# Optimization experiments

Hardware: AMD Instinct MI355X
Metric: run time of the kernel (lower is better)

The kernel has to match this reference:

```python
import jax, jax.numpy as jnp
import numpy as np

B, N, D, H = 2, 2048, 1024, 16
DK = D // H
SCALE = DK ** -0.5


def setup_inputs() -> dict:
    key = jax.random.key(0)
    ks = jax.random.split(key, 11)
    s = D ** -0.5
    return {
        "q": jax.random.normal(ks[0], (B, N, D), jnp.float32),
        "k": jax.random.normal(ks[1], (B, N, D), jnp.float32),
        "v": jax.random.normal(ks[2], (B, N, D), jnp.float32),
        "Wq": jax.random.normal(ks[3], (D, D), jnp.float32) * s,
        "bq": jnp.zeros((D,), jnp.float32),
        "Wk": jax.random.normal(ks[4], (D, D), jnp.float32) * s,
        "bk": jnp.zeros((D,), jnp.float32),
        "Wv": jax.random.normal(ks[5], (D, D), jnp.float32) * s,
        "bv": jnp.zeros((D,), jnp.float32),
        "Wo": jax.random.normal(ks[6], (D, D), jnp.float32) * s,
        "bo": jnp.zeros((D,), jnp.float32),
    }


def _split_heads(x):
    # [b, n, h*d] -> [b, h, n, d]
    b, n, _ = x.shape
    return x.reshape(b, n, H, DK).transpose(0, 2, 1, 3)


def reference(q, k, v, Wq, bq, Wk, bk, Wv, bv, Wo, bo):
    qh = _split_heads(q @ Wq.T + bq)
    kh = _split_heads(k @ Wk.T + bk)
    vh = _split_heads(v @ Wv.T + bv)
    dots = jnp.einsum('bhid,bhjd->bhij', qh, kh) * SCALE
    attn = jax.nn.softmax(dots, axis=-1)
    out = jnp.einsum('bhij,bhjd->bhid', attn, vh)
    out = out.transpose(0, 2, 1, 3).reshape(q.shape[0], q.shape[1], D)
    return out @ Wo.T + bo
```

## Files before the change

kernel.cpp:

```cpp
#include <hip/hip_runtime.h>
#include <hip/hip_bf16.h>
#include <cstdint>
#include <cstddef>

#define BB 2
#define NN 2048
#define DD 1024
#define HH 16
#define DKK 64
#define SCALE 0.125f
#define LOG2E 1.4426950408889634f

typedef __bf16 bf16;
typedef __bf16 bf16x4 __attribute__((ext_vector_type(4)));
typedef __bf16 bf16x8 __attribute__((ext_vector_type(8)));
typedef float f32x4 __attribute__((ext_vector_type(4)));
typedef short s16x4 __attribute__((ext_vector_type(4)));

#define GLD(gp, lp)                                                            \
  __builtin_amdgcn_global_load_lds(                                            \
      (const __attribute__((address_space(1))) void*)(gp),                     \
      (__attribute__((address_space(3))) void*)(lp), 16, 0, 0)

struct CvtArgs { const float* s[7]; bf16* d[7]; int n[7]; };

__global__ void k_cvt(CvtArgs a) {
  const int seg = blockIdx.y;
  const float* __restrict__ s = a.s[seg];
  bf16* __restrict__ d = a.d[seg];
  int i = (blockIdx.x * 256 + threadIdx.x) * 8;
  if (i >= a.n[seg]) return;
  float4 f0 = *(const float4*)(s + i);
  float4 f1 = *(const float4*)(s + i + 4);
  bf16x8 o;
  o[0] = (bf16)f0.x; o[1] = (bf16)f0.y; o[2] = (bf16)f0.z; o[3] = (bf16)f0.w;
  o[4] = (bf16)f1.x; o[5] = (bf16)f1.y; o[6] = (bf16)f1.z; o[7] = (bf16)f1.w;
  *(bf16x8*)(d + i) = o;
}

template <int BN>
__device__ __forceinline__ void gemm_body(
    const bf16* __restrict__ A, const bf16* __restrict__ W,
    const float* __restrict__ bias, bf16* __restrict__ outB,
    float* __restrict__ outF, int mode, float oscale, int m0, int n0) {
  const int K = 1024;
  constexpr int NI = BN / 32;
  constexpr int BI = BN * 8 / 256;
  __shared__ bf16 lA[128 * 64];
  __shared__ bf16 lB[BN * 64];
  const int t = threadIdx.x;
  const int lane = t & 63, quad = lane >> 4, l16 = lane & 15, w = t >> 6;
  const int wm = (w >> 1) * 64, wn = (w & 1) * (BN / 2);

  f32x4 acc[4][NI] = {};

  const bf16* gA[4]; const bf16* gB[BI];
#pragma unroll
  for (int i4 = 0; i4 < 4; i4++) {
    int i = i4 * 256 + t;
    int r = i >> 3, c = (i & 7) ^ (r & 7);
    gA[i4] = A + (size_t)(m0 + r) * K + c * 8;
  }
#pragma unroll
  for (int i4 = 0; i4 < BI; i4++) {
    int i = i4 * 256 + t;
    int r = i >> 3, c = (i & 7) ^ (r & 7);
    gB[i4] = W + (size_t)(n0 + r) * K + c * 8;
  }

  for (int kb = 0; kb < K; kb += 64) {
    __syncthreads();
#pragma unroll
    for (int i4 = 0; i4 < 4; i4++) GLD(gA[i4] + kb, lA + (i4 * 256 + t) * 8);
#pragma unroll
    for (int i4 = 0; i4 < BI; i4++) GLD(gB[i4] + kb, lB + (i4 * 256 + t) * 8);
    __syncthreads();

#pragma unroll
    for (int kb2 = 0; kb2 < 2; kb2++) {
      bf16x8 af[4], bfr[NI];
      const int ch = ((kb2 * 4 + quad) ^ (l16 & 7)) * 8;
#pragma unroll
      for (int i = 0; i < 4; i++)
        af[i] = *(const bf16x8*)(lA + (wm + i * 16 + l16) * 64 + ch);
#pragma unroll
      for (int i = 0; i < NI; i++)
        bfr[i] = *(const bf16x8*)(lB + (wn + i * 16 + l16) * 64 + ch);
#pragma unroll
      for (int mi = 0; mi < 4; mi++)
#pragma unroll
        for (int ni = 0; ni < NI; ni++)
          acc[mi][ni] = __builtin_amdgcn_mfma_f32_16x16x32_bf16(
              af[mi], bfr[ni], acc[mi][ni], 0, 0, 0);
    }
  }

  if (mode == 2) {
    __syncthreads();
    bf16* scr = (w < 2 ? lA : lB) + (w & 1) * 4096;
#pragma unroll
    for (int ni = 0; ni < NI; ni++) {
      int c = ni * 16 + l16;
      float bs = bias[n0 + wn + c];
#pragma unroll
      for (int mi = 0; mi < 4; mi++) {
        int u = (mi * 2 + (quad >> 1)) ^ (c & 7);
        bf16x4 pv;
#pragma unroll
        for (int r = 0; r < 4; r++)
          pv[r] = (bf16)((acc[mi][ni][r] + bs) * oscale);
        *(bf16x4*)(scr + c * 64 + u * 8 + (quad & 1) * 4) = pv;
      }
    }
    __syncthreads();
    {
      const int gm0 = m0 + wm;
      const int b = gm0 >> 11, row0 = gm0 & 2047;
#pragma unroll
      for (int it = 0; it < 8; it++) {
        int c = it * 8 + (lane >> 3);
        int u = (lane & 7) ^ (lane >> 3);
        bf16x8 val = *(const bf16x8*)(scr + c * 64 + u * 8);
        int gn = n0 + wn + c;
        int h = gn >> 6, dk = gn & 63;
        *(bf16x8*)(outB + ((size_t)(b * HH + h) * DKK + dk) * NN + row0 +
                   (lane & 7) * 8) = val;
      }
    }
    return;
  }
#pragma unroll
  for (int mi = 0; mi < 4; mi++) {
#pragma unroll
    for (int ni = 0; ni < NI; ni++) {
#pragma unroll
      for (int r = 0; r < 4; r++) {
        int gm = m0 + wm + mi * 16 + quad * 4 + r;
        int gn = n0 + wn + ni * 16 + l16;
        float v = (acc[mi][ni][r] + bias[gn]) * oscale;
        if (mode == 3) {
          outF[(size_t)gm * 1024 + gn] = v;
        } else {
          int b = gm >> 11, row = gm & 2047;
          int h = gn >> 6, dk = gn & 63;
          outB[((size_t)(b * HH + h) * NN + row) * DKK + dk] = (bf16)v;
        }
      }
    }
  }
}

struct QkvArgs {
  const bf16* A; const bf16* W; const float* b[3]; bf16* o[3]; float sc0;
};

__global__ __launch_bounds__(256, 3) void k_qkv(QkvArgs g) {
  const int z = blockIdx.z;
  gemm_body<128>(g.A + (size_t)z * 4194304, g.W + (size_t)z * 1048576,
                 g.b[z], g.o[z], nullptr, z == 2 ? 2 : 0,
                 z == 0 ? g.sc0 : 1.0f, blockIdx.x * 128, blockIdx.y * 128);
}

__global__ __launch_bounds__(256, 4) void k_oproj(
    const bf16* __restrict__ A, const bf16* __restrict__ W,
    const float* __restrict__ bias, float* __restrict__ out) {
  gemm_body<64>(A, W, bias, nullptr, out, 3, 1.0f, blockIdx.x * 128,
                blockIdx.y * 64);
}

__global__ __launch_bounds__(512, 4) void k_attn(
    const bf16* __restrict__ Qp, const bf16* __restrict__ Kp,
    const bf16* __restrict__ Vt, bf16* __restrict__ Ao) {
  __shared__ bf16 lK[2][128 * 64];
  __shared__ bf16 lV[2][64 * 128];
  const int t = threadIdx.x;
  const int lane = t & 63, quad = lane >> 4, l16 = lane & 15, w = t >> 6;
  const int wq = w & 3;
  const int kh = w >> 2;
  const int bh = blockIdx.x;
  const int qt = blockIdx.y;
  const bf16* Qb = Qp + (size_t)bh * NN * DKK;
  const bf16* Kb = Kp + (size_t)bh * NN * DKK;
  const bf16* Vb = Vt + (size_t)bh * DKK * NN;

  const int qr0 = qt * 128 + wq * 32;
  bf16x8 qf[2][2];
#pragma unroll
  for (int j = 0; j < 2; j++)
#pragma unroll
    for (int kq = 0; kq < 2; kq++)
      qf[j][kq] = *(const bf16x8*)(Qb + (size_t)(qr0 + j * 16 + l16) * DKK +
                                   kq * 32 + quad * 8);

  float lj[2] = {0.f, 0.f};
  f32x4 oaccT[2][4] = {};

  const bf16* gK[2]; const bf16* gV[2];
#pragma unroll
  for (int i2 = 0; i2 < 2; i2++) {
    int i = i2 * 512 + t;
    int rK = i >> 3, cK = (i & 7) ^ (rK & 7);
    gK[i2] = Kb + (size_t)rK * DKK + cK * 8;
    int rV = i >> 4, cV = (i & 15) ^ (rV & 15);
    gV[i2] = Vb + (size_t)rV * NN + cV * 8;
  }
  const int swzK0 = (quad ^ (l16 & 7)) * 8;
  const int swzK1 = ((4 + quad) ^ (l16 & 7)) * 8;

#pragma unroll
  for (int i2 = 0; i2 < 2; i2++) {
    GLD(gK[i2], &lK[0][(i2 * 512 + t) * 8]);
    GLD(gV[i2], &lV[0][(i2 * 512 + t) * 8]);
  }

  int p = 0;
  for (int kt = 0; kt < NN; kt += 128) {
    __syncthreads();
    if (kt + 128 < NN) {
#pragma unroll
      for (int i2 = 0; i2 < 2; i2++) {
        GLD(gK[i2] + (size_t)(kt + 128) * DKK, &lK[p ^ 1][(i2 * 512 + t) * 8]);
        GLD(gV[i2] + (kt + 128), &lV[p ^ 1][(i2 * 512 + t) * 8]);
      }
    }

    f32x4 s[2][4];
#pragma unroll
    for (int tt = 0; tt < 4; tt++) {
      const bf16* kbase = &lK[p][((kh * 4 + tt) * 16 + l16) * 64];
      bf16x8 kf0 = *(const bf16x8*)(kbase + swzK0);
      bf16x8 kf1 = *(const bf16x8*)(kbase + swzK1);
#pragma unroll
      for (int j = 0; j < 2; j++) {
        f32x4 z = {0.f, 0.f, 0.f, 0.f};
        z = __builtin_amdgcn_mfma_f32_16x16x32_bf16(kf0, qf[j][0], z, 0, 0, 0);
        z = __builtin_amdgcn_mfma_f32_16x16x32_bf16(kf1, qf[j][1], z, 0, 0, 0);
        s[j][tt] = z;
      }
    }

    s16x4 pa[2][4];
#pragma unroll
    for (int j = 0; j < 2; j++) {
      float rs = 0.f;
#pragma unroll
      for (int tt = 0; tt < 4; tt++) {
        bf16x4 pb;
#pragma unroll
        for (int r = 0; r < 4; r++) {
          float pe = __builtin_amdgcn_exp2f(s[j][tt][r]);
          rs += pe;
          pb[r] = (bf16)pe;
        }
        pa[j][tt] = __builtin_bit_cast(s16x4, pb);
      }
      lj[j] += rs;
    }

#pragma unroll
    for (int tt = 0; tt < 4; tt++) {
#pragma unroll
      for (int ni = 0; ni < 4; ni++) {
        int rv = ni * 16 + l16;
        int cc = kh * 8 + 2 * tt + (quad >> 1);
        const bf16* vaddr =
            &lV[p][rv * 128 + ((cc ^ l16) * 8) + (quad & 1) * 4];
        s16x4 vb = __builtin_bit_cast(s16x4, *(const bf16x4*)vaddr);
#pragma unroll
        for (int j = 0; j < 2; j++)
          oaccT[j][ni] = __builtin_amdgcn_mfma_f32_16x16x16bf16_1k(
              vb, pa[j][tt], oaccT[j][ni], 0, 0, 0);
      }
    }
    p ^= 1;
  }

  __syncthreads();
  float* redO = (float*)&lK[0][0];
  float* redL = (float*)&lV[0][0];
  const int R = wq * 64 + lane;
  if (kh == 1) {
#pragma unroll
    for (int j = 0; j < 2; j++)
#pragma unroll
      for (int ni = 0; ni < 4; ni++)
        *(f32x4*)(redO + ((j * 4 + ni) * 1024 + R * 4)) = oaccT[j][ni];
    redL[R * 2 + 0] = lj[0];
    redL[R * 2 + 1] = lj[1];
  }
  __syncthreads();
  if (kh == 0) {
#pragma unroll
    for (int j = 0; j < 2; j++)
#pragma unroll
      for (int ni = 0; ni < 4; ni++)
        oaccT[j][ni] += *(const f32x4*)(redO + ((j * 4 + ni) * 1024 + R * 4));
    lj[0] += redL[R * 2 + 0];
    lj[1] += redL[R * 2 + 1];

    const int b = bh >> 4, h = bh & 15;
#pragma unroll
    for (int j = 0; j < 2; j++) {
      float l = lj[j];
      l += __shfl_xor(l, 16);
      l += __shfl_xor(l, 32);
      const float inv = 1.0f / l;
      bf16* dst = Ao + ((size_t)(b * NN) + qr0 + j * 16 + l16) * DD +
                  h * DKK + quad * 4;
#pragma unroll
      for (int ni = 0; ni < 4; ni++) {
        bf16x4 ov;
#pragma unroll
        for (int r = 0; r < 4; r++) ov[r] = (bf16)(oaccT[j][ni][r] * inv);
        *(bf16x4*)(dst + ni * 16) = ov;
      }
    }
  }
}

extern "C" void kernel_launch(void* const* d_in, const int* in_sizes, int n_in,
                              void* d_out, int out_size, void* d_ws,
                              size_t ws_size, hipStream_t stream) {
  const float* qin = (const float*)d_in[0];
  const float* kin = (const float*)d_in[1];
  const float* vin = (const float*)d_in[2];
  const float* Wq = (const float*)d_in[3];
  const float* bq = (const float*)d_in[4];
  const float* Wk = (const float*)d_in[5];
  const float* bk = (const float*)d_in[6];
  const float* Wv = (const float*)d_in[7];
  const float* bv = (const float*)d_in[8];
  const float* Wo = (const float*)d_in[9];
  const float* bo = (const float*)d_in[10];
  float* out = (float*)d_out;

  const int MN = BB * NN * DD;
  const int WNel = DD * DD;
  bf16* ws = (bf16*)d_ws;
  bf16* Xb = ws;
  bf16* Wb = Xb + 3 * MN;
  bf16* Qp = Wb + 4 * WNel;
  bf16* Kp = Qp + MN;
  bf16* Vt = Kp + MN;
  bf16* Ao = Xb;

  CvtArgs ca{{qin, kin, vin, Wq, Wk, Wv, Wo},
             {Xb, Xb + MN, Xb + 2 * MN, Wb, Wb + WNel, Wb + 2 * WNel,
              Wb + 3 * WNel},
             {MN, MN, MN, WNel, WNel, WNel, WNel}};
  k_cvt<<<dim3(2048, 7), 256, 0, stream>>>(ca);

  QkvArgs g{Xb, Wb, {bq, bk, bv}, {Qp, Kp, Vt}, SCALE * LOG2E};
  k_qkv<<<dim3(32, 8, 3), 256, 0, stream>>>(g);
  k_attn<<<dim3(32, 16), 512, 0, stream>>>(Qp, Kp, Vt, Ao);
  k_oproj<<<dim3(32, 16), 256, 0, stream>>>(Ao, Wb + 3 * WNel, bo, out);
}
```

Before: 211.7 us.

## Load V fragments directly from global memory instead of staging through LDS

The attention kernel stops staging V tiles in shared memory. Each lane now reads its bf16x4 V fragments straight from global (transposed V layout) inside the PV loop. This halves LDS usage, which allows raising the launch-bounds occupancy hint to 8 blocks and adds a small separate buffer for the row-sum reduction. The trade-off is that V reads become uncoalesced 8-byte global loads with no prefetch. Each K/V tile is re-read by several waves through the cache, which may expose memory latency in the inner loop.

```diff
diff --git a/kernel.cpp b/kernel.cpp
--- a/kernel.cpp
+++ b/kernel.cpp
@@ -168,11 +168,11 @@
                 blockIdx.y * 64);
 }
 
-__global__ __launch_bounds__(512, 4) void k_attn(
+__global__ __launch_bounds__(512, 8) void k_attn(
     const bf16* __restrict__ Qp, const bf16* __restrict__ Kp,
     const bf16* __restrict__ Vt, bf16* __restrict__ Ao) {
   __shared__ bf16 lK[2][128 * 64];
-  __shared__ bf16 lV[2][64 * 128];
+  __shared__ float redL2[512];
   const int t = threadIdx.x;
   const int lane = t & 63, quad = lane >> 4, l16 = lane & 15, w = t >> 6;
   const int wq = w & 3;
@@ -195,33 +195,31 @@
   float lj[2] = {0.f, 0.f};
   f32x4 oaccT[2][4] = {};
 
-  const bf16* gK[2]; const bf16* gV[2];
+  const bf16* gK[2];
 #pragma unroll
   for (int i2 = 0; i2 < 2; i2++) {
     int i = i2 * 512 + t;
     int rK = i >> 3, cK = (i & 7) ^ (rK & 7);
     gK[i2] = Kb + (size_t)rK * DKK + cK * 8;
-    int rV = i >> 4, cV = (i & 15) ^ (rV & 15);
-    gV[i2] = Vb + (size_t)rV * NN + cV * 8;
   }
   const int swzK0 = (quad ^ (l16 & 7)) * 8;
   const int swzK1 = ((4 + quad) ^ (l16 & 7)) * 8;
 
-#pragma unroll
-  for (int i2 = 0; i2 < 2; i2++) {
-    GLD(gK[i2], &lK[0][(i2 * 512 + t) * 8]);
-    GLD(gV[i2], &lV[0][(i2 * 512 + t) * 8]);
-  }
+  const bf16* pV[4];
+#pragma unroll
+  for (int ni = 0; ni < 4; ni++)
+    pV[ni] = Vb + (size_t)(ni * 16 + l16) * NN + kh * 64 + quad * 4;
+
+#pragma unroll
+  for (int i2 = 0; i2 < 2; i2++) GLD(gK[i2], &lK[0][(i2 * 512 + t) * 8]);
 
   int p = 0;
   for (int kt = 0; kt < NN; kt += 128) {
     __syncthreads();
     if (kt + 128 < NN) {
 #pragma unroll
-      for (int i2 = 0; i2 < 2; i2++) {
+      for (int i2 = 0; i2 < 2; i2++)
         GLD(gK[i2] + (size_t)(kt + 128) * DKK, &lK[p ^ 1][(i2 * 512 + t) * 8]);
-        GLD(gV[i2] + (kt + 128), &lV[p ^ 1][(i2 * 512 + t) * 8]);
-      }
     }
 
     f32x4 s[2][4];
@@ -258,26 +256,24 @@
     }
 
 #pragma unroll
-    for (int tt = 0; tt < 4; tt++) {
-#pragma unroll
-      for (int ni = 0; ni < 4; ni++) {
-        int rv = ni * 16 + l16;
-        int cc = kh * 8 + 2 * tt + (quad >> 1);
-        const bf16* vaddr =
-            &lV[p][rv * 128 + ((cc ^ l16) * 8) + (quad & 1) * 4];
-        s16x4 vb = __builtin_bit_cast(s16x4, *(const bf16x4*)vaddr);
+    for (int ni = 0; ni < 4; ni++) {
+      s16x4 vb[4];
+#pragma unroll
+      for (int tt = 0; tt < 4; tt++)
+        vb[tt] = __builtin_bit_cast(
+            s16x4, *(const bf16x4*)(pV[ni] + kt + tt * 16));
+#pragma unroll
+      for (int tt = 0; tt < 4; tt++)
 #pragma unroll
         for (int j = 0; j < 2; j++)
           oaccT[j][ni] = __builtin_amdgcn_mfma_f32_16x16x16bf16_1k(
-              vb, pa[j][tt], oaccT[j][ni], 0, 0, 0);
-      }
+              vb[tt], pa[j][tt], oaccT[j][ni], 0, 0, 0);
     }
     p ^= 1;
   }
 
   __syncthreads();
   float* redO = (float*)&lK[0][0];
-  float* redL = (float*)&lV[0][0];
   const int R = wq * 64 + lane;
   if (kh == 1) {
 #pragma unroll
@@ -285,8 +281,8 @@
 #pragma unroll
       for (int ni = 0; ni < 4; ni++)
         *(f32x4*)(redO + ((j * 4 + ni) * 1024 + R * 4)) = oaccT[j][ni];
-    redL[R * 2 + 0] = lj[0];
-    redL[R * 2 + 1] = lj[1];
+    redL2[R * 2 + 0] = lj[0];
+    redL2[R * 2 + 1] = lj[1];
   }
   __syncthreads();
   if (kh == 0) {
@@ -295,8 +291,8 @@
 #pragma unroll
       for (int ni = 0; ni < 4; ni++)
         oaccT[j][ni] += *(const f32x4*)(redO + ((j * 4 + ni) * 1024 + R * 4));
-    lj[0] += redL[R * 2 + 0];
-    lj[1] += redL[R * 2 + 1];
+    lj[0] += redL2[R * 2 + 0];
+    lj[1] += redL2[R * 2 + 1];
 
     const int b = bh >> 4, h = bh & 15;
 #pragma unroll
```

After: 456.1 us. +115.4%, slower.
